# Optimization experiments

Hardware: AMD Instinct MI355X
Metric: run time of the kernel (lower is better)

The kernel has to match this reference:

```python
import jax, jax.numpy as jnp
import numpy as np

E = 8           # num_experts
K = 2           # num_experts_per_tok
D = 1024        # hidden_size
F = 2048        # intermediate_dim
B, S = 1, 2048  # batch, seq_len


def setup_inputs() -> dict:
    key = jax.random.key(0)
    k0, k1, k2, k3, k4, k5 = jax.random.split(key, 6)
    hidden_states = jax.random.normal(k0, (B, S, D), dtype=jnp.float32)
    topk_weights = jax.random.uniform(k1, (B * S, K), dtype=jnp.float32)
    topk_ids = jax.random.randint(k2, (B * S, K), 0, E, dtype=jnp.int32)
    scale = 0.02
    wi_0 = jax.random.normal(k3, (E, D, F), dtype=jnp.float32) * scale
    wi_1 = jax.random.normal(k4, (E, D, F), dtype=jnp.float32) * scale
    wo = jax.random.normal(k5, (E, F, D), dtype=jnp.float32) * scale
    return {"hidden_states": hidden_states, "topk_weights": topk_weights,
            "topk_ids": topk_ids, "wi_0": wi_0, "wi_1": wi_1, "wo": wo}


def _gmm(x, w, group_sizes):
    """Grouped matmul: rows of x are sorted by expert; group_sizes[e] rows use w[e].
    Small fixed loop over experts (E=8); rows not owned by expert e are masked out."""
    n_e = w.shape[0]
    expert_of_row = jnp.repeat(jnp.arange(n_e), group_sizes,
                               total_repeat_length=x.shape[0])  # [M]
    out = jnp.zeros((x.shape[0], w.shape[2]), dtype=x.dtype)
    for e in range(n_e):
        out = out + jnp.where((expert_of_row == e)[:, None], x @ w[e], 0.0)
    return out


def _moe_forward(hidden_states, topk_weights, topk_ids, wi_0, wi_1, wo):
    b, s, d = hidden_states.shape
    k = topk_ids.shape[1]
    n_e = wi_0.shape[0]
    x2d = hidden_states.reshape(b * s, d)

    # ---- permute: sort expanded tokens by selected expert (stable) ----
    flat_experts = jnp.ravel(topk_ids)                       # [T*K]
    sort_idx = jnp.argsort(flat_experts, stable=True)        # [T*K]
    sorted_rows = sort_idx // k                              # source token per row
    x_sorted = jnp.take(x2d, sorted_rows, axis=0)            # [T*K, D]
    group_sizes = jnp.bincount(flat_experts, length=n_e)     # [E]

    # ---- grouped GEMMs with SwiGLU (gate * up, then down) ----
    g0 = _gmm(x_sorted, wi_0, group_sizes)                   # [T*K, F]
    g1 = _gmm(x_sorted, wi_1, group_sizes)                   # [T*K, F]
    h = jax.nn.silu(g0) * g1                                 # fused SiLU-gate
    y = _gmm(h, wo, group_sizes)                             # [T*K, D]

    # ---- unpermute and combine with routing weights (fp32 accum) ----
    unsort_idx = jnp.argsort(sort_idx, stable=True)
    y = jnp.take(y, unsort_idx, axis=0).reshape(b * s, k, d)
    out = jnp.einsum('bke,bk->be', y.astype(jnp.float32),
                     topk_weights.astype(jnp.float32))
    return out.reshape(b, s, d)


def reference(hidden_states, topk_weights, topk_ids, wi_0, wi_1, wo):
    return _moe_forward(hidden_states, topk_weights, topk_ids, wi_0, wi_1, wo)
```

## Files before the change

kernel.cpp:

```cpp
#include <hip/hip_runtime.h>
#include <hip/hip_bf16.h>


#define D_DIM 1024
#define F_DIM 2048
#define ROWS 4096
#define MAXTILE 40
#define LDK 72

using f32x4 = __attribute__((ext_vector_type(4))) float;
using s16x8 = __attribute__((ext_vector_type(8))) short;

__device__ __forceinline__ unsigned pack_trunc(float lo, float hi) {
  return (__float_as_uint(lo) >> 16) | (__float_as_uint(hi) & 0xffff0000u);
}
__device__ __forceinline__ unsigned short bf_rn(float f) {
  unsigned u = __float_as_uint(f);
  u += 0x7fffu + ((u >> 16) & 1u);
  return (unsigned short)(u >> 16);
}
__device__ __forceinline__ unsigned pack_rn(float lo, float hi) {
  return (unsigned)bf_rn(lo) | ((unsigned)bf_rn(hi) << 16);
}

typedef const __attribute__((address_space(1))) void* gp_t;
typedef __attribute__((address_space(3))) void* lp_t;
__device__ __forceinline__ void load16(const void* g, void* l) {
  __builtin_amdgcn_global_load_lds((gp_t)g, (lp_t)l, 16, 0, 0);
}

__global__ __launch_bounds__(512) void route_kernel(const int* __restrict__ ids,
                                                    int* __restrict__ sorted_flat,
                                                    int* __restrict__ unsort,
                                                    int* __restrict__ tile_meta) {
  __shared__ int sid[ROWS];
  __shared__ int cnt[8];
  __shared__ int off[9];
  const int tid = threadIdx.x;
#pragma unroll
  for (int j = 0; j < 2; j++) {
    int idx = tid + j * 512;
    *(int4*)&sid[idx * 4] = *(const int4*)&ids[idx * 4];
  }
  __syncthreads();
  const int w = tid >> 6, lane = tid & 63;
  int c = 0;
  for (int base = 0; base < ROWS; base += 64)
    c += __popcll(__ballot(sid[base + lane] == w));
  if (lane == 0) cnt[w] = c;
  __syncthreads();
  if (tid == 0) {
    int o = 0;
    for (int e = 0; e < 8; e++) { off[e] = o; o += cnt[e]; }
    off[8] = o;
    int nT = 0;
    for (int e = 0; e < 8; e++) {
      for (int r0 = off[e]; r0 < off[e + 1]; r0 += 128) {
        tile_meta[1 + 3 * nT] = r0;
        tile_meta[2 + 3 * nT] = off[e + 1];
        tile_meta[3 + 3 * nT] = e;
        nT++;
      }
    }
    tile_meta[0] = nT;
  }
  __syncthreads();
  int pos = off[w];
  const unsigned long long below = (1ull << lane) - 1ull;
  for (int base = 0; base < ROWS; base += 64) {
    unsigned long long m = __ballot(sid[base + lane] == w);
    if (sid[base + lane] == w) {
      int p = pos + __popcll(m & below);
      sorted_flat[p] = base + lane;
      unsort[base + lane] = p;
    }
    pos += __popcll(m);
  }
}

__global__ void zero_kernel(float4* __restrict__ p, int n4) {
  int i = blockIdx.x * blockDim.x + threadIdx.x;
  if (i < n4) p[i] = float4{0.f, 0.f, 0.f, 0.f};
}

__global__ __launch_bounds__(256) void convT_lds(
    const float* __restrict__ wi0, const float* __restrict__ wi1,
    const float* __restrict__ wo, unsigned short* __restrict__ w0T,
    unsigned short* __restrict__ w1T, unsigned short* __restrict__ woT) {
  __shared__ unsigned t[64 * 65];
  const int z = blockIdx.y;
  const int which = z >> 3, e = z & 7;
  const float* S;
  unsigned short* Dp;
  int Kd, Nd, nbits;
  if (which == 0)      { S = wi0; Dp = w0T; Kd = D_DIM; Nd = F_DIM; nbits = 5; }
  else if (which == 1) { S = wi1; Dp = w1T; Kd = D_DIM; Nd = F_DIM; nbits = 5; }
  else                 { S = wo;  Dp = woT; Kd = F_DIM; Nd = D_DIM; nbits = 4; }
  S  += (size_t)e * Kd * Nd;
  Dp += (size_t)e * Kd * Nd;
  const int n0 = (blockIdx.x & ((1 << nbits) - 1)) * 64;
  const int k0 = (blockIdx.x >> nbits) * 128;
  const int tid = threadIdx.x;
  const int nb = (tid & 15) * 4;
  float4 v[4][2];
#pragma unroll
  for (int i = 0; i < 4; i++) {
    const int kp = (tid >> 4) + i * 16;
    const float* p = S + (size_t)(k0 + 2 * kp) * Nd + n0 + nb;
    v[i][0] = *(const float4*)p;
    v[i][1] = *(const float4*)(p + Nd);
  }
#pragma unroll
  for (int i = 0; i < 4; i++) {
    const int kp = (tid >> 4) + i * 16;
    t[(nb + 0) * 65 + kp] = pack_rn(v[i][0].x, v[i][1].x);
    t[(nb + 1) * 65 + kp] = pack_rn(v[i][0].y, v[i][1].y);
    t[(nb + 2) * 65 + kp] = pack_rn(v[i][0].z, v[i][1].z);
    t[(nb + 3) * 65 + kp] = pack_rn(v[i][0].w, v[i][1].w);
  }
  __syncthreads();
  const int c = tid & 15;
#pragma unroll
  for (int j = 0; j < 4; j++) {
    const int n = (tid >> 4) + j * 16;
    const unsigned* q = &t[n * 65 + c * 4];
    uint4 o = make_uint4(q[0], q[1], q[2], q[3]);
    *(uint4*)(Dp + (size_t)(n0 + n) * Kd + k0 + c * 8) = o;
  }
}

__global__ __launch_bounds__(256) void gather_kernel(const float* __restrict__ x,
                                                     const int* __restrict__ sorted_flat,
                                                     unsigned short* __restrict__ xs) {
  const int r = blockIdx.x;
  const int tok = sorted_flat[r] >> 1;
  const float4 v = *(const float4*)(x + (size_t)tok * D_DIM + threadIdx.x * 4);
  *(uint2*)(xs + (size_t)r * D_DIM + threadIdx.x * 4) =
      make_uint2(pack_rn(v.x, v.y), pack_rn(v.z, v.w));
}

__device__ __forceinline__ int sw(int row, int chunk) {
  return row * 64 + ((chunk ^ (row & 7)) << 3);
}

__global__ __launch_bounds__(256, 3) void gemm1_kernel(
    const unsigned short* __restrict__ xs, const unsigned short* __restrict__ w0T,
    const unsigned short* __restrict__ w1T, const int* __restrict__ tile_meta,
    unsigned short* __restrict__ h) {
  __shared__ unsigned short As[128 * 64];
  __shared__ unsigned short B0s[64 * 64];
  __shared__ unsigned short B1s[64 * 64];
  const int tile = blockIdx.x;
  if (tile >= tile_meta[0]) return;
  const int row0 = tile_meta[1 + 3 * tile];
  const int rowEnd = tile_meta[2 + 3 * tile];
  const int e = tile_meta[3 + 3 * tile];
  const int n0 = blockIdx.y * 64;
  const unsigned short* W0 = w0T + ((size_t)e * F_DIM + n0) * D_DIM;
  const unsigned short* W1 = w1T + ((size_t)e * F_DIM + n0) * D_DIM;

  const int tid = threadIdx.x;
  const int lane = tid & 63, wv = tid >> 6;
  const int wm = (wv & 1) * 64, wn = (wv >> 1) * 32;
  const int lm = lane & 15, lq = lane >> 4;
  const int srow = lane >> 3;
  const int skk = ((lane & 7) ^ srow) << 3;

  f32x4 acc0[4][2], acc1[4][2];
#pragma unroll
  for (int i = 0; i < 4; i++)
#pragma unroll
    for (int j = 0; j < 2; j++) { acc0[i][j] = 0.f; acc1[i][j] = 0.f; }

  for (int k0 = 0; k0 < D_DIM; k0 += 64) {
    __syncthreads();
#pragma unroll
    for (int r = 0; r < 4; r++) {
      const int c = r * 4 + wv;
      const int m = c * 8 + srow;
      int mc = row0 + m; if (mc > ROWS - 1) mc = ROWS - 1;
      load16(xs + (size_t)mc * D_DIM + k0 + skk, (char*)As + c * 1024);
    }
#pragma unroll
    for (int r = 0; r < 2; r++) {
      const int c = r * 4 + wv;
      const int m = c * 8 + srow;
      load16(W0 + (size_t)m * D_DIM + k0 + skk, (char*)B0s + c * 1024);
      load16(W1 + (size_t)m * D_DIM + k0 + skk, (char*)B1s + c * 1024);
    }
    __syncthreads();
#pragma unroll
    for (int ks = 0; ks < 64; ks += 32) {
      const int cb = (ks >> 3) + lq;
      s16x8 af[4], b0[2], b1[2];
#pragma unroll
      for (int t = 0; t < 4; t++)
        af[t] = *(const s16x8*)&As[sw(wm + t * 16 + lm, cb)];
#pragma unroll
      for (int t = 0; t < 2; t++) {
        b0[t] = *(const s16x8*)&B0s[sw(wn + t * 16 + lm, cb)];
        b1[t] = *(const s16x8*)&B1s[sw(wn + t * 16 + lm, cb)];
      }
#pragma unroll
      for (int im = 0; im < 4; im++)
#pragma unroll
        for (int in = 0; in < 2; in++) {
          acc0[im][in] = __builtin_amdgcn_mfma_f32_16x16x32_bf16(
              af[im], b0[in], acc0[im][in], 0, 0, 0);
          acc1[im][in] = __builtin_amdgcn_mfma_f32_16x16x32_bf16(
              af[im], b1[in], acc1[im][in], 0, 0, 0);
        }
    }
  }
#pragma unroll
  for (int im = 0; im < 4; im++) {
    int gmB = row0 + wm + im * 16 + lq * 4;
#pragma unroll
    for (int in = 0; in < 2; in++) {
      int gn = n0 + wn + in * 16 + lm;
#pragma unroll
      for (int r = 0; r < 4; r++) {
        int gm = gmB + r;
        if (gm < rowEnd) {
          float g = acc0[im][in][r];
          float s = g / (1.f + __expf(-g));
          h[(size_t)gm * F_DIM + gn] = bf_rn(s * acc1[im][in][r]);
        }
      }
    }
  }
}

__global__ __launch_bounds__(256, 4) void gemm2_kernel(
    const unsigned short* __restrict__ h, const unsigned short* __restrict__ woT,
    const int* __restrict__ tile_meta, float* __restrict__ y) {
  __shared__ unsigned short As[128 * 64];
  __shared__ unsigned short Bs[64 * 64];
  const int tile = blockIdx.x;
  if (tile >= tile_meta[0]) return;
  const int row0 = tile_meta[1 + 3 * tile];
  const int rowEnd = tile_meta[2 + 3 * tile];
  const int e = tile_meta[3 + 3 * tile];
  const int n0 = blockIdx.y * 64;
  const unsigned short* W = woT + ((size_t)e * D_DIM + n0) * F_DIM;

  const int tid = threadIdx.x;
  const int lane = tid & 63, wv = tid >> 6;
  const int wm = (wv & 1) * 64, wn = (wv >> 1) * 32;
  const int lm = lane & 15, lq = lane >> 4;
  const int srow = lane >> 3;
  const int skk = ((lane & 7) ^ srow) << 3;

  f32x4 acc[4][2];
#pragma unroll
  for (int i = 0; i < 4; i++)
#pragma unroll
    for (int j = 0; j < 2; j++) acc[i][j] = 0.f;

  for (int k0 = 0; k0 < F_DIM; k0 += 64) {
    __syncthreads();
#pragma unroll
    for (int r = 0; r < 4; r++) {
      const int c = r * 4 + wv;
      const int m = c * 8 + srow;
      int mc = row0 + m; if (mc > ROWS - 1) mc = ROWS - 1;
      load16(h + (size_t)mc * F_DIM + k0 + skk, (char*)As + c * 1024);
    }
#pragma unroll
    for (int r = 0; r < 2; r++) {
      const int c = r * 4 + wv;
      const int m = c * 8 + srow;
      load16(W + (size_t)m * F_DIM + k0 + skk, (char*)Bs + c * 1024);
    }
    __syncthreads();
#pragma unroll
    for (int ks = 0; ks < 64; ks += 32) {
      const int cb = (ks >> 3) + lq;
      s16x8 af[4], bf[2];
#pragma unroll
      for (int t = 0; t < 4; t++)
        af[t] = *(const s16x8*)&As[sw(wm + t * 16 + lm, cb)];
#pragma unroll
      for (int t = 0; t < 2; t++)
        bf[t] = *(const s16x8*)&Bs[sw(wn + t * 16 + lm, cb)];
#pragma unroll
      for (int im = 0; im < 4; im++)
#pragma unroll
        for (int in = 0; in < 2; in++)
          acc[im][in] = __builtin_amdgcn_mfma_f32_16x16x32_bf16(
              af[im], bf[in], acc[im][in], 0, 0, 0);
    }
  }
#pragma unroll
  for (int im = 0; im < 4; im++) {
    int gmB = row0 + wm + im * 16 + lq * 4;
#pragma unroll
    for (int in = 0; in < 2; in++) {
      int gn = n0 + wn + in * 16 + lm;
#pragma unroll
      for (int r = 0; r < 4; r++) {
        int gm = gmB + r;
        if (gm < rowEnd) y[(size_t)gm * D_DIM + gn] = acc[im][in][r];
      }
    }
  }
}

__global__ __launch_bounds__(256) void combine_kernel(const float* __restrict__ y,
                                                      const float* __restrict__ tw,
                                                      const int* __restrict__ unsort,
                                                      float* __restrict__ out) {
  const int tkn = blockIdx.x;
  const int r0 = unsort[2 * tkn], r1 = unsort[2 * tkn + 1];
  const float w0 = tw[2 * tkn], w1 = tw[2 * tkn + 1];
  const int c = threadIdx.x * 4;
  float4 a = *(const float4*)(y + (size_t)r0 * D_DIM + c);
  float4 b = *(const float4*)(y + (size_t)r1 * D_DIM + c);
  float4 o = {w0 * a.x + w1 * b.x, w0 * a.y + w1 * b.y,
              w0 * a.z + w1 * b.z, w0 * a.w + w1 * b.w};
  *(float4*)(out + (size_t)tkn * D_DIM + c) = o;
}

__device__ __forceinline__ void stage_bt(const float* __restrict__ Wt, int ldw,
                                         unsigned short* Bs, int tid) {
#pragma unroll
  for (int it = 0; it < 4; it++) {
    const int kp = (tid & 7) + it * 8;
    const int nq = tid >> 3;
    const float* p = Wt + (size_t)(2 * kp) * ldw + nq * 4;
    const float4 va = *(const float4*)p;
    const float4 vb = *(const float4*)(p + ldw);
    unsigned short* b = Bs + (nq * 4) * LDK + 2 * kp;
    *(unsigned*)(b)           = pack_trunc(va.x, vb.x);
    *(unsigned*)(b + LDK)     = pack_trunc(va.y, vb.y);
    *(unsigned*)(b + 2 * LDK) = pack_trunc(va.z, vb.z);
    *(unsigned*)(b + 3 * LDK) = pack_trunc(va.w, vb.w);
  }
}

__global__ __launch_bounds__(256, 2) void gemm1_fb(
    const float* __restrict__ x, const float* __restrict__ wi0,
    const float* __restrict__ wi1, const int* __restrict__ sorted_flat,
    const int* __restrict__ tile_meta, unsigned short* __restrict__ h) {
  __shared__ unsigned short As[128 * LDK];
  __shared__ unsigned short B0s[128 * LDK];
  __shared__ unsigned short B1s[128 * LDK];
  __shared__ int tok[128];
  const int tile = blockIdx.x;
  if (tile >= tile_meta[0]) return;
  const int row0 = tile_meta[1 + 3 * tile];
  const int rowEnd = tile_meta[2 + 3 * tile];
  const int e = tile_meta[3 + 3 * tile];
  const int n0 = blockIdx.y * 128;
  const float* W0 = wi0 + (size_t)e * D_DIM * F_DIM;
  const float* W1 = wi1 + (size_t)e * D_DIM * F_DIM;
  const int tid = threadIdx.x;
  if (tid < 128) {
    int r = row0 + tid; if (r > ROWS - 1) r = ROWS - 1;
    tok[tid] = sorted_flat[r] >> 1;
  }
  f32x4 acc0[4][4], acc1[4][4];
#pragma unroll
  for (int i = 0; i < 4; i++)
#pragma unroll
    for (int j = 0; j < 4; j++) { acc0[i][j] = 0.f; acc1[i][j] = 0.f; }
  const int lane = tid & 63, wv = tid >> 6;
  const int wm = (wv & 1) * 64, wn = (wv >> 1) * 64;
  const int lm = lane & 15, lq = lane >> 4;
  for (int k0 = 0; k0 < D_DIM; k0 += 64) {
    __syncthreads();
#pragma unroll
    for (int i = 0; i < 8; i++) {
      int idx = tid + i * 256;
      int m = idx >> 4, kq = idx & 15;
      float4 v = *(const float4*)(x + (size_t)tok[m] * D_DIM + k0 + kq * 4);
      *(uint2*)&As[m * LDK + kq * 4] =
          make_uint2(pack_trunc(v.x, v.y), pack_trunc(v.z, v.w));
    }
    stage_bt(W0 + (size_t)k0 * F_DIM + n0, F_DIM, B0s, tid);
    stage_bt(W1 + (size_t)k0 * F_DIM + n0, F_DIM, B1s, tid);
    __syncthreads();
#pragma unroll
    for (int ks = 0; ks < 64; ks += 32) {
      s16x8 af[4], b0[4], b1[4];
#pragma unroll
      for (int t = 0; t < 4; t++) {
        af[t] = *(const s16x8*)&As[(wm + t * 16 + lm) * LDK + ks + lq * 8];
        b0[t] = *(const s16x8*)&B0s[(wn + t * 16 + lm) * LDK + ks + lq * 8];
        b1[t] = *(const s16x8*)&B1s[(wn + t * 16 + lm) * LDK + ks + lq * 8];
      }
#pragma unroll
      for (int im = 0; im < 4; im++)
#pragma unroll
        for (int in = 0; in < 4; in++) {
          acc0[im][in] = __builtin_amdgcn_mfma_f32_16x16x32_bf16(
              af[im], b0[in], acc0[im][in], 0, 0, 0);
          acc1[im][in] = __builtin_amdgcn_mfma_f32_16x16x32_bf16(
              af[im], b1[in], acc1[im][in], 0, 0, 0);
        }
    }
  }
#pragma unroll
  for (int im = 0; im < 4; im++) {
    int gmB = row0 + wm + im * 16 + lq * 4;
#pragma unroll
    for (int in = 0; in < 4; in++) {
      int gn = n0 + wn + in * 16 + lm;
#pragma unroll
      for (int r = 0; r < 4; r++) {
        int gm = gmB + r;
        if (gm < rowEnd) {
          float g = acc0[im][in][r];
          float s = g / (1.f + __expf(-g));
          h[(size_t)gm * F_DIM + gn] = bf_rn(s * acc1[im][in][r]);
        }
      }
    }
  }
}

__global__ __launch_bounds__(256, 3) void gemm2_fb(
    const unsigned short* __restrict__ h, const float* __restrict__ wo,
    const float* __restrict__ tw, const int* __restrict__ sorted_flat,
    const int* __restrict__ tile_meta, float* __restrict__ out) {
  __shared__ unsigned short As[128 * LDK];
  __shared__ unsigned short Bs[128 * LDK];
  __shared__ int sTok[128];
  __shared__ float sWgt[128];
  const int tile = blockIdx.x;
  if (tile >= tile_meta[0]) return;
  const int row0 = tile_meta[1 + 3 * tile];
  const int rowEnd = tile_meta[2 + 3 * tile];
  const int e = tile_meta[3 + 3 * tile];
  const int n0 = blockIdx.y * 128;
  const float* W = wo + (size_t)e * F_DIM * D_DIM;
  const int tid = threadIdx.x;
  if (tid < 128) {
    int r = row0 + tid; if (r > ROWS - 1) r = ROWS - 1;
    int fl = sorted_flat[r];
    sTok[tid] = fl >> 1;
    sWgt[tid] = tw[fl];
  }
  f32x4 acc[4][4];
#pragma unroll
  for (int i = 0; i < 4; i++)
#pragma unroll
    for (int j = 0; j < 4; j++) acc[i][j] = 0.f;
  const int lane = tid & 63, wv = tid >> 6;
  const int wm = (wv & 1) * 64, wn = (wv >> 1) * 64;
  const int lm = lane & 15, lq = lane >> 4;
  for (int k0 = 0; k0 < F_DIM; k0 += 64) {
    __syncthreads();
#pragma unroll
    for (int i = 0; i < 8; i++) {
      int idx = tid + i * 256;
      int m = idx >> 4, kq = idx & 15;
      int gm = row0 + m; if (gm > ROWS - 1) gm = ROWS - 1;
      *(uint2*)&As[m * LDK + kq * 4] =
          *(const uint2*)(h + (size_t)gm * F_DIM + k0 + kq * 4);
    }
    stage_bt(W + (size_t)k0 * D_DIM + n0, D_DIM, Bs, tid);
    __syncthreads();
#pragma unroll
    for (int ks = 0; ks < 64; ks += 32) {
      s16x8 af[4], bf[4];
#pragma unroll
      for (int t = 0; t < 4; t++) {
        af[t] = *(const s16x8*)&As[(wm + t * 16 + lm) * LDK + ks + lq * 8];
        bf[t] = *(const s16x8*)&Bs[(wn + t * 16 + lm) * LDK + ks + lq * 8];
      }
#pragma unroll
      for (int im = 0; im < 4; im++)
#pragma unroll
        for (int in = 0; in < 4; in++)
          acc[im][in] = __builtin_amdgcn_mfma_f32_16x16x32_bf16(
              af[im], bf[in], acc[im][in], 0, 0, 0);
    }
  }
#pragma unroll
  for (int im = 0; im < 4; im++) {
    int lrB = wm + im * 16 + lq * 4;
#pragma unroll
    for (int in = 0; in < 4; in++) {
      int gn = n0 + wn + in * 16 + lm;
#pragma unroll
      for (int r = 0; r < 4; r++) {
        int lr = lrB + r;
        int gm = row0 + lr;
        if (gm < rowEnd)
          atomicAdd(out + (size_t)sTok[lr] * D_DIM + gn, sWgt[lr] * acc[im][in][r]);
      }
    }
  }
}

extern "C" void kernel_launch(void* const* d_in, const int* in_sizes, int n_in,
                              void* d_out, int out_size, void* d_ws, size_t ws_size,
                              hipStream_t stream) {
  const float* x   = (const float*)d_in[0];
  const float* tw  = (const float*)d_in[1];
  const int*   ids = (const int*)d_in[2];
  const float* wi0 = (const float*)d_in[3];
  const float* wi1 = (const float*)d_in[4];
  const float* wo  = (const float*)d_in[5];
  float* out = (float*)d_out;

  int* tile_meta = (int*)d_ws;
  int* sorted_flat = tile_meta + 256;
  int* unsort = sorted_flat + ROWS;

  const size_t MB = 1024 * 1024;
  const size_t XS_OFF = 64 * 1024;
  const size_t H_OFF  = XS_OFF + 8 * MB;
  const size_t W0_OFF = H_OFF + 16 * MB;
  const size_t W1_OFF = W0_OFF + 32 * MB;
  const size_t WO_OFF = W1_OFF + 32 * MB;
  const size_t NEED   = WO_OFF + 32 * MB;

  route_kernel<<<1, 512, 0, stream>>>(ids, sorted_flat, unsort, tile_meta);
  if (ws_size >= NEED) {
    unsigned short* xs  = (unsigned short*)((char*)d_ws + XS_OFF);
    unsigned short* h   = (unsigned short*)((char*)d_ws + H_OFF);
    unsigned short* w0T = (unsigned short*)((char*)d_ws + W0_OFF);
    unsigned short* w1T = (unsigned short*)((char*)d_ws + W1_OFF);
    unsigned short* woT = (unsigned short*)((char*)d_ws + WO_OFF);
    float* y = (float*)((char*)d_ws + W0_OFF);

    convT_lds<<<dim3(256, 24), 256, 0, stream>>>(wi0, wi1, wo, w0T, w1T, woT);
    gather_kernel<<<ROWS, 256, 0, stream>>>(x, sorted_flat, xs);
    gemm1_kernel<<<dim3(MAXTILE, F_DIM / 64), 256, 0, stream>>>(xs, w0T, w1T,
                                                                tile_meta, h);
    gemm2_kernel<<<dim3(MAXTILE, D_DIM / 64), 256, 0, stream>>>(h, woT,
                                                                tile_meta, y);
    combine_kernel<<<ROWS / 2, 256, 0, stream>>>(y, tw, unsort, out);
  } else {
    unsigned short* h = (unsigned short*)((char*)d_ws + XS_OFF);
    zero_kernel<<<(out_size / 4 + 255) / 256, 256, 0, stream>>>((float4*)out,
                                                                out_size / 4);
    gemm1_fb<<<dim3(MAXTILE, F_DIM / 128), 256, 0, stream>>>(x, wi0, wi1,
                                                             sorted_flat,
                                                             tile_meta, h);
    gemm2_fb<<<dim3(MAXTILE, D_DIM / 128), 256, 0, stream>>>(h, wo, tw,
                                                             sorted_flat,
                                                             tile_meta, out);
  }
}
```

Measured before the change: 323.5 us.

## Fuse fp32 weight conversion into GEMM B-tile staging, drop transpose kernel

Removes the separate weight transpose/bf16 conversion kernel and instead has each GEMM block load fp32 weights directly, round to bf16 and write them into swizzled LDS. This saves a full pass over 192MB of fp32 weights plus a 96MB bf16 write and re-read. The cost is that weight tiles are now re-read in fp32 (twice the bytes) by every row tile of an expert, with synchronous register-staged loads instead of async LDS loads. gemm2's occupancy hint drops from 4 to 3.

```diff
diff --git a/kernel.cpp b/kernel.cpp
--- a/kernel.cpp
+++ b/kernel.cpp
@@ -83,52 +83,6 @@
   if (i < n4) p[i] = float4{0.f, 0.f, 0.f, 0.f};
 }
 
-__global__ __launch_bounds__(256) void convT_lds(
-    const float* __restrict__ wi0, const float* __restrict__ wi1,
-    const float* __restrict__ wo, unsigned short* __restrict__ w0T,
-    unsigned short* __restrict__ w1T, unsigned short* __restrict__ woT) {
-  __shared__ unsigned t[64 * 65];
-  const int z = blockIdx.y;
-  const int which = z >> 3, e = z & 7;
-  const float* S;
-  unsigned short* Dp;
-  int Kd, Nd, nbits;
-  if (which == 0)      { S = wi0; Dp = w0T; Kd = D_DIM; Nd = F_DIM; nbits = 5; }
-  else if (which == 1) { S = wi1; Dp = w1T; Kd = D_DIM; Nd = F_DIM; nbits = 5; }
-  else                 { S = wo;  Dp = woT; Kd = F_DIM; Nd = D_DIM; nbits = 4; }
-  S  += (size_t)e * Kd * Nd;
-  Dp += (size_t)e * Kd * Nd;
-  const int n0 = (blockIdx.x & ((1 << nbits) - 1)) * 64;
-  const int k0 = (blockIdx.x >> nbits) * 128;
-  const int tid = threadIdx.x;
-  const int nb = (tid & 15) * 4;
-  float4 v[4][2];
-#pragma unroll
-  for (int i = 0; i < 4; i++) {
-    const int kp = (tid >> 4) + i * 16;
-    const float* p = S + (size_t)(k0 + 2 * kp) * Nd + n0 + nb;
-    v[i][0] = *(const float4*)p;
-    v[i][1] = *(const float4*)(p + Nd);
-  }
-#pragma unroll
-  for (int i = 0; i < 4; i++) {
-    const int kp = (tid >> 4) + i * 16;
-    t[(nb + 0) * 65 + kp] = pack_rn(v[i][0].x, v[i][1].x);
-    t[(nb + 1) * 65 + kp] = pack_rn(v[i][0].y, v[i][1].y);
-    t[(nb + 2) * 65 + kp] = pack_rn(v[i][0].z, v[i][1].z);
-    t[(nb + 3) * 65 + kp] = pack_rn(v[i][0].w, v[i][1].w);
-  }
-  __syncthreads();
-  const int c = tid & 15;
-#pragma unroll
-  for (int j = 0; j < 4; j++) {
-    const int n = (tid >> 4) + j * 16;
-    const unsigned* q = &t[n * 65 + c * 4];
-    uint4 o = make_uint4(q[0], q[1], q[2], q[3]);
-    *(uint4*)(Dp + (size_t)(n0 + n) * Kd + k0 + c * 8) = o;
-  }
-}
-
 __global__ __launch_bounds__(256) void gather_kernel(const float* __restrict__ x,
                                                      const int* __restrict__ sorted_flat,
                                                      unsigned short* __restrict__ xs) {
@@ -143,9 +97,27 @@
   return row * 64 + ((chunk ^ (row & 7)) << 3);
 }
 
+__device__ __forceinline__ void stage_bfp32(const float* __restrict__ Wt, int ldw,
+                                            unsigned* __restrict__ Bu,
+                                            int kp, int nq) {
+#pragma unroll
+  for (int it = 0; it < 2; it++) {
+    const int kpp = kp + it * 16;
+    const float* p = Wt + (size_t)(2 * kpp) * ldw + nq * 4;
+    const float4 va = *(const float4*)p;
+    const float4 vb = *(const float4*)(p + ldw);
+    const int ch = kpp >> 2, ql = kpp & 3;
+    const int nb = nq * 4;
+    Bu[(nb + 0) * 32 + ((ch ^ ((nb + 0) & 7)) << 2) + ql] = pack_rn(va.x, vb.x);
+    Bu[(nb + 1) * 32 + ((ch ^ ((nb + 1) & 7)) << 2) + ql] = pack_rn(va.y, vb.y);
+    Bu[(nb + 2) * 32 + ((ch ^ ((nb + 2) & 7)) << 2) + ql] = pack_rn(va.z, vb.z);
+    Bu[(nb + 3) * 32 + ((ch ^ ((nb + 3) & 7)) << 2) + ql] = pack_rn(va.w, vb.w);
+  }
+}
+
 __global__ __launch_bounds__(256, 3) void gemm1_kernel(
-    const unsigned short* __restrict__ xs, const unsigned short* __restrict__ w0T,
-    const unsigned short* __restrict__ w1T, const int* __restrict__ tile_meta,
+    const unsigned short* __restrict__ xs, const float* __restrict__ wi0,
+    const float* __restrict__ wi1, const int* __restrict__ tile_meta,
     unsigned short* __restrict__ h) {
   __shared__ unsigned short As[128 * 64];
   __shared__ unsigned short B0s[64 * 64];
@@ -156,8 +128,8 @@
   const int rowEnd = tile_meta[2 + 3 * tile];
   const int e = tile_meta[3 + 3 * tile];
   const int n0 = blockIdx.y * 64;
-  const unsigned short* W0 = w0T + ((size_t)e * F_DIM + n0) * D_DIM;
-  const unsigned short* W1 = w1T + ((size_t)e * F_DIM + n0) * D_DIM;
+  const float* W0 = wi0 + (size_t)e * D_DIM * F_DIM + n0;
+  const float* W1 = wi1 + (size_t)e * D_DIM * F_DIM + n0;
 
   const int tid = threadIdx.x;
   const int lane = tid & 63, wv = tid >> 6;
@@ -165,6 +137,7 @@
   const int lm = lane & 15, lq = lane >> 4;
   const int srow = lane >> 3;
   const int skk = ((lane & 7) ^ srow) << 3;
+  const int kp = tid & 15, nq = tid >> 4;
 
   f32x4 acc0[4][2], acc1[4][2];
 #pragma unroll
@@ -181,13 +154,8 @@
       int mc = row0 + m; if (mc > ROWS - 1) mc = ROWS - 1;
       load16(xs + (size_t)mc * D_DIM + k0 + skk, (char*)As + c * 1024);
     }
-#pragma unroll
-    for (int r = 0; r < 2; r++) {
-      const int c = r * 4 + wv;
-      const int m = c * 8 + srow;
-      load16(W0 + (size_t)m * D_DIM + k0 + skk, (char*)B0s + c * 1024);
-      load16(W1 + (size_t)m * D_DIM + k0 + skk, (char*)B1s + c * 1024);
-    }
+    stage_bfp32(W0 + (size_t)k0 * F_DIM, F_DIM, (unsigned*)B0s, kp, nq);
+    stage_bfp32(W1 + (size_t)k0 * F_DIM, F_DIM, (unsigned*)B1s, kp, nq);
     __syncthreads();
 #pragma unroll
     for (int ks = 0; ks < 64; ks += 32) {
@@ -231,8 +199,8 @@
   }
 }
 
-__global__ __launch_bounds__(256, 4) void gemm2_kernel(
-    const unsigned short* __restrict__ h, const unsigned short* __restrict__ woT,
+__global__ __launch_bounds__(256, 3) void gemm2_kernel(
+    const unsigned short* __restrict__ h, const float* __restrict__ wo,
     const int* __restrict__ tile_meta, float* __restrict__ y) {
   __shared__ unsigned short As[128 * 64];
   __shared__ unsigned short Bs[64 * 64];
@@ -242,7 +210,7 @@
   const int rowEnd = tile_meta[2 + 3 * tile];
   const int e = tile_meta[3 + 3 * tile];
   const int n0 = blockIdx.y * 64;
-  const unsigned short* W = woT + ((size_t)e * D_DIM + n0) * F_DIM;
+  const float* W = wo + (size_t)e * F_DIM * D_DIM + n0;
 
   const int tid = threadIdx.x;
   const int lane = tid & 63, wv = tid >> 6;
@@ -250,6 +218,7 @@
   const int lm = lane & 15, lq = lane >> 4;
   const int srow = lane >> 3;
   const int skk = ((lane & 7) ^ srow) << 3;
+  const int kp = tid & 15, nq = tid >> 4;
 
   f32x4 acc[4][2];
 #pragma unroll
@@ -266,12 +235,7 @@
       int mc = row0 + m; if (mc > ROWS - 1) mc = ROWS - 1;
       load16(h + (size_t)mc * F_DIM + k0 + skk, (char*)As + c * 1024);
     }
-#pragma unroll
-    for (int r = 0; r < 2; r++) {
-      const int c = r * 4 + wv;
-      const int m = c * 8 + srow;
-      load16(W + (size_t)m * F_DIM + k0 + skk, (char*)Bs + c * 1024);
-    }
+    stage_bfp32(W + (size_t)k0 * D_DIM, D_DIM, (unsigned*)Bs, kp, nq);
     __syncthreads();
 #pragma unroll
     for (int ks = 0; ks < 64; ks += 32) {
@@ -512,25 +476,19 @@
   const size_t MB = 1024 * 1024;
   const size_t XS_OFF = 64 * 1024;
   const size_t H_OFF  = XS_OFF + 8 * MB;
-  const size_t W0_OFF = H_OFF + 16 * MB;
-  const size_t W1_OFF = W0_OFF + 32 * MB;
-  const size_t WO_OFF = W1_OFF + 32 * MB;
-  const size_t NEED   = WO_OFF + 32 * MB;
+  const size_t Y_OFF  = H_OFF + 16 * MB;
+  const size_t NEED   = Y_OFF + 16 * MB;
 
   route_kernel<<<1, 512, 0, stream>>>(ids, sorted_flat, unsort, tile_meta);
   if (ws_size >= NEED) {
-    unsigned short* xs  = (unsigned short*)((char*)d_ws + XS_OFF);
-    unsigned short* h   = (unsigned short*)((char*)d_ws + H_OFF);
-    unsigned short* w0T = (unsigned short*)((char*)d_ws + W0_OFF);
-    unsigned short* w1T = (unsigned short*)((char*)d_ws + W1_OFF);
-    unsigned short* woT = (unsigned short*)((char*)d_ws + WO_OFF);
-    float* y = (float*)((char*)d_ws + W0_OFF);
-
-    convT_lds<<<dim3(256, 24), 256, 0, stream>>>(wi0, wi1, wo, w0T, w1T, woT);
+    unsigned short* xs = (unsigned short*)((char*)d_ws + XS_OFF);
+    unsigned short* h  = (unsigned short*)((char*)d_ws + H_OFF);
+    float* y = (float*)((char*)d_ws + Y_OFF);
+
     gather_kernel<<<ROWS, 256, 0, stream>>>(x, sorted_flat, xs);
-    gemm1_kernel<<<dim3(MAXTILE, F_DIM / 64), 256, 0, stream>>>(xs, w0T, w1T,
+    gemm1_kernel<<<dim3(MAXTILE, F_DIM / 64), 256, 0, stream>>>(xs, wi0, wi1,
                                                                 tile_meta, h);
-    gemm2_kernel<<<dim3(MAXTILE, D_DIM / 64), 256, 0, stream>>>(h, woT,
+    gemm2_kernel<<<dim3(MAXTILE, D_DIM / 64), 256, 0, stream>>>(h, wo,
                                                                 tile_meta, y);
     combine_kernel<<<ROWS / 2, 256, 0, stream>>>(y, tw, unsort, out);
   } else {
```

Result: slower. 394.7 us (+22.0%).
